# Optimization experiments

Measured on AMD Instinct MI355X. Metric: run time of the kernel, lower is better.

The kernel has to match this reference:

```python
import jax, jax.numpy as jnp
import numpy as np

B = 2
H = 256; Wd = 256; C = 128; S = 16        # image dims, channels, split_size
G = (H // S) * (Wd // S)                  # 256 heads (spatial groups)
N = S * S                                 # 256 patches per head
CI = C // 2                               # 64 channels per branch (gmlp input)
EI = 6                                    # inner gMLP expansion (MabGmlpBlock default e)
F1 = CI * EI                              # 384 = LocallyConnected expansion width
HF = F1 // 2                              # 192 = u/v split width
EPS = 1e-3                                # keras LayerNormalization default epsilon


def layer_norm(x, g, b):
    m = jnp.mean(x, axis=-1, keepdims=True)
    v = jnp.var(x, axis=-1, keepdims=True)
    return (x - m) * jax.lax.rsqrt(v + EPS) * g + b


def make_blocks(x):
    # 'B (H b1) (W b2) C -> B (H W) (b1 b2) C'
    b_, _, _, c_ = x.shape
    x = x.reshape(b_, H // S, S, Wd // S, S, c_)
    return x.transpose(0, 1, 3, 2, 4, 5).reshape(b_, G, N, c_)


def recon_blocks(x):
    # 'B (H W) (b1 b2) C -> B (H b1) (W b2) C'
    b_, _, _, c_ = x.shape
    x = x.reshape(b_, H // S, Wd // S, S, S, c_)
    return x.transpose(0, 1, 3, 2, 4, 5).reshape(b_, H, Wd, c_)


def recon_grids(x):
    # 'B (H W) (d1 d2) C -> B (d1 H) (d2 W) C'
    b_, _, _, c_ = x.shape
    x = x.reshape(b_, H // S, Wd // S, S, S, c_)
    return x.transpose(0, 3, 1, 4, 2, 5).reshape(b_, H, Wd, c_)


def gmlp(x, ln2_g, ln2_b, W1, b1, ln3_g, ln3_b, Wsgu, bsgu, W2, b2):
    # x: [B, G, N, CI]; all heads share weights -> batched einsum over (B, G)
    y = layer_norm(x, ln2_g, ln2_b)
    # LocallyConnected1D kernel_size=1: per-patch distinct weight [N, CI, F1]
    y = jax.nn.gelu(jnp.einsum('bgnc,ncf->bgnf', y, W1) + b1, approximate=False)
    u, v = jnp.split(y, 2, axis=-1)                      # [B,G,N,HF] each
    u = layer_norm(u, ln3_g, ln3_b)
    u = jnp.swapaxes(u, -1, -2)                          # [B,G,HF,N]
    # spatial gating: per-channel distinct [N->N] mixing, bias init ones
    u = jnp.einsum('bgcn,cnm->bgcm', u, Wsgu) + bsgu
    u = jnp.swapaxes(u, -1, -2)                          # [B,G,N,HF]
    return jnp.einsum('bgnc,ncf->bgnf', u * v, W2) + b2 + x


def setup_inputs() -> dict:
    key = jax.random.key(0)
    ks = jax.random.split(key, 8)
    x = jax.random.normal(ks[0], (B, H, Wd, C), jnp.float32)
    W_proj = jax.random.normal(ks[1], (C, C), jnp.float32) / np.sqrt(C).astype(np.float32)
    b_proj = jnp.zeros((C,), jnp.float32)
    W1 = jax.random.normal(ks[2], (N, CI, F1), jnp.float32) / np.sqrt(CI).astype(np.float32)
    b1 = jnp.zeros((N, F1), jnp.float32)
    Wsgu = jax.random.normal(ks[3], (HF, N, N), jnp.float32) * 0.001  # truncated_normal(0.001) approx
    bsgu = jnp.ones((HF, N), jnp.float32)                             # bias_initializer=ones
    W2 = jax.random.normal(ks[4], (N, HF, CI), jnp.float32) / np.sqrt(HF).astype(np.float32)
    b2 = jnp.zeros((N, CI), jnp.float32)
    return {
        'x': x,
        'ln1_g': jnp.ones((C,), jnp.float32), 'ln1_b': jnp.zeros((C,), jnp.float32),
        'W_proj': W_proj, 'b_proj': b_proj,
        'ln2_g': jnp.ones((CI,), jnp.float32), 'ln2_b': jnp.zeros((CI,), jnp.float32),
        'W1': W1, 'b1': b1,
        'ln3_g': jnp.ones((HF,), jnp.float32), 'ln3_b': jnp.zeros((HF,), jnp.float32),
        'Wsgu': Wsgu, 'bsgu': bsgu,
        'W2': W2, 'b2': b2,
    }


def reference(x, ln1_g, ln1_b, W_proj, b_proj, ln2_g, ln2_b, W1, b1,
              ln3_g, ln3_b, Wsgu, bsgu, W2, b2):
    y = layer_norm(x, ln1_g, ln1_b)
    y = jax.nn.gelu(y @ W_proj + b_proj, approximate=False)   # Dense(c*e), e=1
    local, glob = jnp.split(y, 2, axis=-1)                    # [B,H,W,CI] each
    g_args = (ln2_g, ln2_b, W1, b1, ln3_g, ln3_b, Wsgu, bsgu, W2, b2)
    local = recon_grids(gmlp(make_blocks(local), *g_args))    # multi-axis: block in, grid out
    glob = recon_blocks(gmlp(make_blocks(glob), *g_args))
    out = jnp.concatenate([local, glob], axis=-1) + x
    return out, glob
```

## Files before the change

kernel.cpp:

```cpp
#include <hip/hip_runtime.h>


typedef unsigned int uint_t;
typedef unsigned short us_t;
typedef __attribute__((ext_vector_type(8))) short bf16x8;
typedef __attribute__((ext_vector_type(4))) float f32x4;

#define EPSF 1e-3f

__device__ __forceinline__ float b2f(us_t h){ return __uint_as_float(((uint_t)h) << 16); }
__device__ __forceinline__ float lo2f(uint_t u){ return __uint_as_float(u << 16); }
__device__ __forceinline__ float hi2f(uint_t u){ return __uint_as_float(u & 0xFFFF0000u); }
__device__ __forceinline__ us_t f2b(float f){
  uint_t u = __float_as_uint(f);
  uint_t r = (u + 0x7FFFu + ((u >> 16) & 1u)) >> 16;
  return (us_t)r;
}
__device__ __forceinline__ uint_t pack2(float a, float b){
  return (uint_t)f2b(a) | ((uint_t)f2b(b) << 16);
}
__device__ __forceinline__ float gelu_f(float v){
  return 0.5f*v*(1.f + erff(v*0.7071067811865475f));
}

__global__ __launch_bounds__(256) void wprep(const float* __restrict__ Wsgu, us_t* __restrict__ WT){
  __shared__ us_t ls[64*264];
  int t = threadIdx.x;
  int c = blockIdx.x >> 2, kt = blockIdx.x & 3;
  const float* src = Wsgu + ((size_t)c*256 + kt*64)*256;
  #pragma unroll
  for (int i = 0; i < 16; i++){
    int chunk = i*256 + t;
    int kk = chunk >> 6, mm = (chunk & 63) << 2;
    float4 w = *(const float4*)(src + kk*256 + mm);
    *(uint2*)&ls[kk*264 + mm] = make_uint2(pack2(w.x,w.y), pack2(w.z,w.w));
  }
  __syncthreads();
  #pragma unroll
  for (int i = 0; i < 8; i++){
    int chunk = i*256 + t;
    int m = chunk >> 3, kk0 = (chunk & 7) << 3;
    const us_t* sp = &ls[kk0*264 + m];
    uint4 o;
    o.x = (uint_t)sp[0]     | ((uint_t)sp[264]   << 16);
    o.y = (uint_t)sp[2*264] | ((uint_t)sp[3*264] << 16);
    o.z = (uint_t)sp[4*264] | ((uint_t)sp[5*264] << 16);
    o.w = (uint_t)sp[6*264] | ((uint_t)sp[7*264] << 16);
    *(uint4*)(WT + ((size_t)c*256 + m)*256 + kt*64 + kk0) = o;
  }
}

__global__ __launch_bounds__(256) void k1_ln_proj(
    const float* __restrict__ x, const float* __restrict__ g1, const float* __restrict__ b1l,
    const float* __restrict__ Wp, const float* __restrict__ bp, us_t* __restrict__ xin)
{
  __shared__ __align__(16) float xs2[128*40];
  __shared__ __align__(16) us_t Ws[128*128];
  int t = threadIdx.x;
  int p0 = blockIdx.x * 32;

  {
    int pi = t >> 3, c0 = (t & 7) << 4;
    const float* src = x + (size_t)(p0 + pi)*128 + c0;
    float4 d0 = *(const float4*)src;
    float4 d1 = *(const float4*)(src + 4);
    float4 d2 = *(const float4*)(src + 8);
    float4 d3 = *(const float4*)(src + 12);
    float* dst = &xs2[c0*40 + pi];
    dst[0]   = d0.x; dst[40]  = d0.y; dst[80]  = d0.z; dst[120] = d0.w;
    dst[160] = d1.x; dst[200] = d1.y; dst[240] = d1.z; dst[280] = d1.w;
    dst[320] = d2.x; dst[360] = d2.y; dst[400] = d2.z; dst[440] = d2.w;
    dst[480] = d3.x; dst[520] = d3.y; dst[560] = d3.z; dst[600] = d3.w;
  }
  #pragma unroll
  for (int i = 0; i < 16; i++){
    int idx = (i*256 + t)*4;
    float4 w = *(const float4*)(Wp + idx);
    *(uint2*)&Ws[idx] = make_uint2(pack2(w.x,w.y), pack2(w.z,w.w));
  }
  __syncthreads();
  {
    int wv = t >> 6, ln = t & 63;
    float ga = g1[ln], gb = g1[ln+64];
    float ba = b1l[ln], bb = b1l[ln+64];
    for (int k = 0; k < 8; k++){
      int pi = wv*8 + k;
      float a = xs2[ln*40 + pi];
      float c = xs2[(ln+64)*40 + pi];
      float s = a + c, q = a*a + c*c;
      #pragma unroll
      for (int off = 32; off; off >>= 1){ s += __shfl_xor(s, off, 64); q += __shfl_xor(q, off, 64); }
      float m = s*(1.f/128.f);
      float rstd = rsqrtf(q*(1.f/128.f) - m*m + EPSF);
      xs2[ln*40 + pi]      = (a - m)*rstd*ga + ba;
      xs2[(ln+64)*40 + pi] = (c - m)*rstd*gb + bb;
    }
  }
  __syncthreads();
  int cg = t & 31, pg = t >> 5;
  int co0 = cg*4, p00 = pg*4;
  float acc[4][4] = {};
  #pragma unroll 4
  for (int ci = 0; ci < 128; ci++){
    float4 xv = *(const float4*)&xs2[ci*40 + p00];
    uint2 wv2 = *(const uint2*)&Ws[ci*128 + co0];
    float w0 = lo2f(wv2.x), w1 = hi2f(wv2.x), w2 = lo2f(wv2.y), w3 = hi2f(wv2.y);
    acc[0][0] += xv.x*w0; acc[0][1] += xv.x*w1; acc[0][2] += xv.x*w2; acc[0][3] += xv.x*w3;
    acc[1][0] += xv.y*w0; acc[1][1] += xv.y*w1; acc[1][2] += xv.y*w2; acc[1][3] += xv.y*w3;
    acc[2][0] += xv.z*w0; acc[2][1] += xv.z*w1; acc[2][2] += xv.z*w2; acc[2][3] += xv.z*w3;
    acc[3][0] += xv.w*w0; acc[3][1] += xv.w*w1; acc[3][2] += xv.w*w2; acc[3][3] += xv.w*w3;
  }
  float bb0 = bp[co0],   bb1 = bp[co0+1];
  float bb2 = bp[co0+2], bb3 = bp[co0+3];
  int branch = co0 >> 6;
  int c = co0 & 63;
  #pragma unroll
  for (int i = 0; i < 4; i++){
    int p = p0 + p00 + i;
    int b = p >> 16, rem = p & 65535, h = rem >> 8, w = rem & 255;
    int g = ((h >> 4) << 4) | (w >> 4);
    int nn = ((h & 15) << 4) | (w & 15);
    float y0 = gelu_f(acc[i][0] + bb0);
    float y1 = gelu_f(acc[i][1] + bb1);
    float y2 = gelu_f(acc[i][2] + bb2);
    float y3 = gelu_f(acc[i][3] + bb3);
    size_t row = (size_t)branch*512 + (size_t)b*256 + g;
    *(uint2*)(xin + (row*256 + nn)*64 + c) = make_uint2(pack2(y0,y1), pack2(y2,y3));
  }
}

__global__ __launch_bounds__(256) void k2_e1(
    const us_t* __restrict__ xin,
    const float* __restrict__ g2, const float* __restrict__ b2l,
    const float* __restrict__ W1, const float* __restrict__ b1v,
    const float* __restrict__ g3, const float* __restrict__ b3l,
    us_t* __restrict__ u_ln, us_t* __restrict__ vout, int r_base)
{
  __shared__ __align__(16) us_t Wl[64*384];
  __shared__ __align__(16) float xs2[64*36];
  __shared__ float b1s[384];
  int t = threadIdx.x;
  int n = blockIdx.x >> 2, rt = blockIdx.x & 3;

  const float* wsrc = W1 + (size_t)n*24576;
  #pragma unroll
  for (int i = 0; i < 24; i++){
    int idx = (i*256 + t)*4;
    float4 w = *(const float4*)(wsrc + idx);
    *(uint2*)&Wl[idx] = make_uint2(pack2(w.x,w.y), pack2(w.z,w.w));
  }
  if (t < 96){
    float4 d = *(const float4*)(b1v + n*384 + t*4);
    b1s[t*4+0] = d.x; b1s[t*4+1] = d.y; b1s[t*4+2] = d.z; b1s[t*4+3] = d.w;
  }
  {
    int rr = t >> 3, cc0 = (t & 7) << 3;
    uint4 d = *(const uint4*)(xin + ((size_t)(r_base + rt*32 + rr)*256 + n)*64 + cc0);
    float* dst = &xs2[cc0*36 + rr];
    dst[0]    = lo2f(d.x); dst[36]   = hi2f(d.x);
    dst[2*36] = lo2f(d.y); dst[3*36] = hi2f(d.y);
    dst[4*36] = lo2f(d.z); dst[5*36] = hi2f(d.z);
    dst[6*36] = lo2f(d.w); dst[7*36] = hi2f(d.w);
  }
  __syncthreads();
  {
    int wv = t >> 6, ln = t & 63;
    float gch = g2[ln], bch = b2l[ln];
    for (int k = 0; k < 8; k++){
      int row = wv*8 + k;
      float a = xs2[ln*36 + row];
      float s = a, q = a*a;
      #pragma unroll
      for (int off = 32; off; off >>= 1){ s += __shfl_xor(s, off, 64); q += __shfl_xor(q, off, 64); }
      float m = s*(1.f/64.f);
      float rstd = rsqrtf(q*(1.f/64.f) - m*m + EPSF);
      xs2[ln*36 + row] = (a - m)*rstd*gch + bch;
    }
  }
  __syncthreads();
  int fg = t & 31, rg = t >> 5;
  int f0 = fg*12, r00 = rg*4;
  float acc[4][12] = {};
  #pragma unroll 4
  for (int ci = 0; ci < 64; ci++){
    float4 xv = *(const float4*)&xs2[ci*36 + r00];
    const uint2* wp2 = (const uint2*)&Wl[ci*384 + f0];
    uint2 wa = wp2[0], wb = wp2[1], wc = wp2[2];
    float wf[12];
    wf[0]=lo2f(wa.x); wf[1]=hi2f(wa.x); wf[2]=lo2f(wa.y); wf[3]=hi2f(wa.y);
    wf[4]=lo2f(wb.x); wf[5]=hi2f(wb.x); wf[6]=lo2f(wb.y); wf[7]=hi2f(wb.y);
    wf[8]=lo2f(wc.x); wf[9]=hi2f(wc.x); wf[10]=lo2f(wc.y); wf[11]=hi2f(wc.y);
    float xa[4] = {xv.x, xv.y, xv.z, xv.w};
    #pragma unroll
    for (int i = 0; i < 4; i++)
      #pragma unroll
      for (int j = 0; j < 12; j++)
        acc[i][j] += xa[i]*wf[j];
  }
  bool isu = (fg < 16);
  float s4[4], q4[4];
  #pragma unroll
  for (int i = 0; i < 4; i++){
    float s = 0.f, q = 0.f;
    #pragma unroll
    for (int j = 0; j < 12; j++){
      float yv = gelu_f(acc[i][j] + b1s[f0 + j]);
      acc[i][j] = yv;
      s += yv; q += yv*yv;
    }
    s4[i] = isu ? s : 0.f;
    q4[i] = isu ? q : 0.f;
  }
  #pragma unroll
  for (int i = 0; i < 4; i++){
    float s = s4[i], q = q4[i];
    #pragma unroll
    for (int off = 16; off; off >>= 1){ s += __shfl_xor(s, off, 64); q += __shfl_xor(q, off, 64); }
    float m = s*(1.f/192.f);
    s4[i] = m;
    q4[i] = rsqrtf(q*(1.f/192.f) - m*m + EPSF);
  }
  if (isu){
    float gv[12], bv[12];
    #pragma unroll
    for (int j = 0; j < 12; j++){ gv[j] = g3[f0+j]; bv[j] = b3l[f0+j]; }
    #pragma unroll
    for (int i = 0; i < 4; i++){
      int r = rt*32 + r00 + i;
      float m = s4[i], rstd = q4[i];
      uint2* dst = (uint2*)(u_ln + ((size_t)r*256 + n)*192 + f0);
      uint2 o0, o1, o2;
      o0.x = pack2((acc[i][0]-m)*rstd*gv[0]+bv[0],  (acc[i][1]-m)*rstd*gv[1]+bv[1]);
      o0.y = pack2((acc[i][2]-m)*rstd*gv[2]+bv[2],  (acc[i][3]-m)*rstd*gv[3]+bv[3]);
      o1.x = pack2((acc[i][4]-m)*rstd*gv[4]+bv[4],  (acc[i][5]-m)*rstd*gv[5]+bv[5]);
      o1.y = pack2((acc[i][6]-m)*rstd*gv[6]+bv[6],  (acc[i][7]-m)*rstd*gv[7]+bv[7]);
      o2.x = pack2((acc[i][8]-m)*rstd*gv[8]+bv[8],  (acc[i][9]-m)*rstd*gv[9]+bv[9]);
      o2.y = pack2((acc[i][10]-m)*rstd*gv[10]+bv[10],(acc[i][11]-m)*rstd*gv[11]+bv[11]);
      dst[0] = o0; dst[1] = o1; dst[2] = o2;
    }
  } else {
    int fv0 = f0 - 192;
    #pragma unroll
    for (int i = 0; i < 4; i++){
      int r = rt*32 + r00 + i;
      uint2* dst = (uint2*)(vout + ((size_t)r*256 + n)*192 + fv0);
      uint2 o0, o1, o2;
      o0.x = pack2(acc[i][0], acc[i][1]);  o0.y = pack2(acc[i][2], acc[i][3]);
      o1.x = pack2(acc[i][4], acc[i][5]);  o1.y = pack2(acc[i][6], acc[i][7]);
      o2.x = pack2(acc[i][8], acc[i][9]);  o2.y = pack2(acc[i][10], acc[i][11]);
      dst[0] = o0; dst[1] = o1; dst[2] = o2;
    }
  }
}

__global__ __launch_bounds__(256) void t1_transpose(const us_t* __restrict__ u_ln, us_t* __restrict__ uT){
  __shared__ us_t ls[128*194];
  int t = threadIdx.x;
  int r = blockIdx.x >> 1, n0 = (blockIdx.x & 1) << 7;
  #pragma unroll
  for (int i = 0; i < 12; i++){
    int chunk = i*256 + t;
    int nn = chunk/24, c0 = (chunk - nn*24)*8;
    uint4 d = *(const uint4*)(u_ln + ((size_t)r*256 + n0 + nn)*192 + c0);
    us_t* dst = &ls[nn*194 + c0];
    dst[0] = (us_t)d.x; dst[1] = (us_t)(d.x>>16);
    dst[2] = (us_t)d.y; dst[3] = (us_t)(d.y>>16);
    dst[4] = (us_t)d.z; dst[5] = (us_t)(d.z>>16);
    dst[6] = (us_t)d.w; dst[7] = (us_t)(d.w>>16);
  }
  __syncthreads();
  #pragma unroll
  for (int i = 0; i < 12; i++){
    int chunk = i*256 + t;
    int c = chunk >> 4, nn0 = (chunk & 15) << 3;
    const us_t* sp = &ls[nn0*194 + c];
    uint4 o;
    o.x = (uint_t)sp[0]     | ((uint_t)sp[194]   << 16);
    o.y = (uint_t)sp[2*194] | ((uint_t)sp[3*194] << 16);
    o.z = (uint_t)sp[4*194] | ((uint_t)sp[5*194] << 16);
    o.w = (uint_t)sp[6*194] | ((uint_t)sp[7*194] << 16);
    *(uint4*)(uT + ((size_t)c*128 + r)*256 + n0 + nn0) = o;
  }
}

__global__ __launch_bounds__(256) void k3_sgu_mfma(
    const us_t* __restrict__ uT, const us_t* __restrict__ WT,
    const float* __restrict__ bsgu, us_t* __restrict__ sT)
{
  __shared__ __align__(16) us_t As[128*72];
  __shared__ __align__(16) us_t Bs[128*72];
  int t = threadIdx.x;
  int c = blockIdx.x >> 1, mt = blockIdx.x & 1;
  int lane = t & 63, wv = t >> 6;
  int wr0 = (wv >> 1) * 64, wm0 = (wv & 1) * 64;
  int fr = lane & 15, fq = lane >> 4;
  f32x4 acc[4][4] = {};

  const us_t* aSrc = uT + (size_t)c*128*256;
  const us_t* bSrc = WT + ((size_t)(c*256 + mt*128))*256;

  for (int ks = 0; ks < 256; ks += 64){
    #pragma unroll
    for (int i = 0; i < 4; i++){
      int chunk = i*256 + t;
      int rr = chunk >> 3, kk = (chunk & 7) << 3;
      *(uint4*)&As[rr*72 + kk] = *(const uint4*)(aSrc + rr*256 + ks + kk);
      *(uint4*)&Bs[rr*72 + kk] = *(const uint4*)(bSrc + rr*256 + ks + kk);
    }
    __syncthreads();
    #pragma unroll
    for (int s = 0; s < 2; s++){
      int kb = s*32 + fq*8;
      bf16x8 a[4], b[4];
      #pragma unroll
      for (int mi = 0; mi < 4; mi++)
        a[mi] = *(const bf16x8*)&As[(wr0 + mi*16 + fr)*72 + kb];
      #pragma unroll
      for (int ni = 0; ni < 4; ni++)
        b[ni] = *(const bf16x8*)&Bs[(wm0 + ni*16 + fr)*72 + kb];
      #pragma unroll
      for (int mi = 0; mi < 4; mi++)
        #pragma unroll
        for (int ni = 0; ni < 4; ni++)
          acc[mi][ni] = __builtin_amdgcn_mfma_f32_16x16x32_bf16(a[mi], b[ni], acc[mi][ni], 0, 0, 0);
    }
    __syncthreads();
  }
  float bsv[4];
  #pragma unroll
  for (int ni = 0; ni < 4; ni++)
    bsv[ni] = bsgu[c*256 + mt*128 + wm0 + ni*16 + fr];
  #pragma unroll
  for (int mi = 0; mi < 4; mi++){
    #pragma unroll
    for (int i = 0; i < 4; i++){
      int r = wr0 + mi*16 + fq*4 + i;
      us_t* dst = sT + ((size_t)c*128 + r)*256 + mt*128 + wm0 + fr;
      #pragma unroll
      for (int ni = 0; ni < 4; ni++)
        dst[ni*16] = f2b(acc[mi][ni][i] + bsv[ni]);
    }
  }
}

__global__ __launch_bounds__(256) void t2_mul(
    const us_t* __restrict__ sT, const us_t* __restrict__ v, us_t* __restrict__ tout)
{
  __shared__ us_t ls[192*130];
  int t = threadIdx.x;
  int r = blockIdx.x >> 1, m0 = (blockIdx.x & 1) << 7;
  #pragma unroll
  for (int i = 0; i < 12; i++){
    int chunk = i*256 + t;
    int c = chunk >> 4, mm0 = (chunk & 15) << 3;
    uint4 d = *(const uint4*)(sT + ((size_t)c*128 + r)*256 + m0 + mm0);
    us_t* dst = &ls[c*130 + mm0];
    dst[0] = (us_t)d.x; dst[1] = (us_t)(d.x>>16);
    dst[2] = (us_t)d.y; dst[3] = (us_t)(d.y>>16);
    dst[4] = (us_t)d.z; dst[5] = (us_t)(d.z>>16);
    dst[6] = (us_t)d.w; dst[7] = (us_t)(d.w>>16);
  }
  __syncthreads();
  #pragma unroll
  for (int i = 0; i < 12; i++){
    int chunk = i*256 + t;
    int mm = chunk/24, c0 = (chunk - mm*24)*8;
    size_t gidx = ((size_t)r*256 + m0 + mm)*192 + c0;
    uint4 vv = *(const uint4*)(v + gidx);
    const us_t* sp = &ls[c0*130 + mm];
    uint4 o;
    o.x = pack2(b2f(sp[0])*lo2f(vv.x),     b2f(sp[130])*hi2f(vv.x));
    o.y = pack2(b2f(sp[2*130])*lo2f(vv.y), b2f(sp[3*130])*hi2f(vv.y));
    o.z = pack2(b2f(sp[4*130])*lo2f(vv.z), b2f(sp[5*130])*hi2f(vv.z));
    o.w = pack2(b2f(sp[6*130])*lo2f(vv.w), b2f(sp[7*130])*hi2f(vv.w));
    *(uint4*)(tout + gidx) = o;
  }
}

__global__ __launch_bounds__(256) void k4_out(
    const us_t* __restrict__ tbuf, const float* __restrict__ W2,
    const float* __restrict__ b2v, const us_t* __restrict__ xin,
    const float* __restrict__ x, float* __restrict__ out0, float* __restrict__ out1,
    int r_base)
{
  __shared__ __align__(16) us_t W2s[192*64];
  __shared__ __align__(16) us_t ts[192*68];
  int t = threadIdx.x;
  int n = blockIdx.x >> 1, rt = blockIdx.x & 1;
  const float* wsrc = W2 + (size_t)n*12288;
  #pragma unroll
  for (int i = 0; i < 12; i++){
    int idx = (i*256 + t)*4;
    float4 w = *(const float4*)(wsrc + idx);
    *(uint2*)&W2s[idx] = make_uint2(pack2(w.x,w.y), pack2(w.z,w.w));
  }
  #pragma unroll
  for (int i = 0; i < 6; i++){
    int chunk = i*256 + t;
    int rr = chunk/24, ff0 = (chunk - rr*24)*8;
    uint4 d = *(const uint4*)(tbuf + ((size_t)(rt*64 + rr)*256 + n)*192 + ff0);
    us_t* dst = &ts[ff0*68 + rr];
    dst[0]    = (us_t)d.x; dst[68]   = (us_t)(d.x>>16);
    dst[2*68] = (us_t)d.y; dst[3*68] = (us_t)(d.y>>16);
    dst[4*68] = (us_t)d.z; dst[5*68] = (us_t)(d.z>>16);
    dst[6*68] = (us_t)d.w; dst[7*68] = (us_t)(d.w>>16);
  }
  __syncthreads();
  int cg = t & 15, rg = t >> 4;
  int c0 = cg*4, rr0 = rg*4;
  float acc[4][4] = {};
  #pragma unroll 4
  for (int f = 0; f < 192; f++){
    uint2 au = *(const uint2*)&ts[f*68 + rr0];
    uint2 wu = *(const uint2*)&W2s[f*64 + c0];
    float a0 = lo2f(au.x), a1 = hi2f(au.x), a2 = lo2f(au.y), a3 = hi2f(au.y);
    float w0 = lo2f(wu.x), w1 = hi2f(wu.x), w2 = lo2f(wu.y), w3 = hi2f(wu.y);
    acc[0][0] += a0*w0; acc[0][1] += a0*w1; acc[0][2] += a0*w2; acc[0][3] += a0*w3;
    acc[1][0] += a1*w0; acc[1][1] += a1*w1; acc[1][2] += a1*w2; acc[1][3] += a1*w3;
    acc[2][0] += a2*w0; acc[2][1] += a2*w1; acc[2][2] += a2*w2; acc[2][3] += a2*w3;
    acc[3][0] += a3*w0; acc[3][1] += a3*w1; acc[3][2] += a3*w2; acc[3][3] += a3*w3;
  }
  float4 bb = *(const float4*)(b2v + n*64 + c0);
  #pragma unroll
  for (int i = 0; i < 4; i++){
    int rl = rt*64 + rr0 + i;
    int r = r_base + rl;
    int branch = r >> 9, bidx = (r >> 8) & 1, g = r & 255;
    uint2 xi = *(const uint2*)(xin + ((size_t)r*256 + n)*64 + c0);
    float v0 = acc[i][0] + bb.x + lo2f(xi.x);
    float v1 = acc[i][1] + bb.y + hi2f(xi.x);
    float v2 = acc[i][2] + bb.z + lo2f(xi.y);
    float v3 = acc[i][3] + bb.w + hi2f(xi.y);
    int h, w;
    if (branch == 0){ h = ((n >> 4) << 4) | (g >> 4); w = ((n & 15) << 4) | (g & 15); }
    else            { h = ((g >> 4) << 4) | (n >> 4); w = ((g & 15) << 4) | (n & 15); }
    size_t base = (size_t)(bidx*256 + h)*256 + w;
    size_t o0idx = base*128 + (branch << 6) + c0;
    float4 xr = *(const float4*)(x + o0idx);
    *(float4*)(out0 + o0idx) = make_float4(v0 + xr.x, v1 + xr.y, v2 + xr.z, v3 + xr.w);
    if (branch){
      *(float4*)(out1 + base*64 + c0) = make_float4(v0, v1, v2, v3);
    }
  }
}

extern "C" void kernel_launch(void* const* d_in, const int* in_sizes, int n_in,
                              void* d_out, int out_size, void* d_ws, size_t ws_size,
                              hipStream_t stream)
{
  (void)in_sizes; (void)n_in; (void)out_size; (void)ws_size;
  const float* x    = (const float*)d_in[0];
  const float* g1   = (const float*)d_in[1];
  const float* b1l  = (const float*)d_in[2];
  const float* Wp   = (const float*)d_in[3];
  const float* bp   = (const float*)d_in[4];
  const float* g2   = (const float*)d_in[5];
  const float* b2l  = (const float*)d_in[6];
  const float* W1   = (const float*)d_in[7];
  const float* b1v  = (const float*)d_in[8];
  const float* g3   = (const float*)d_in[9];
  const float* b3l  = (const float*)d_in[10];
  const float* Wsgu = (const float*)d_in[11];
  const float* bsgu = (const float*)d_in[12];
  const float* W2   = (const float*)d_in[13];
  const float* b2v  = (const float*)d_in[14];

  float* out0 = (float*)d_out;
  float* out1 = out0 + (size_t)2*256*256*128;

  us_t* ws   = (us_t*)d_ws;
  us_t* xin  = ws;
  us_t* bufA = ws + 16777216;
  us_t* bufV = bufA + 6291456;
  us_t* bufB = bufV + 6291456;
  us_t* WT   = bufB + 6291456;

  wprep      <<<dim3(768),  dim3(256), 0, stream>>>(Wsgu, WT);
  k1_ln_proj <<<dim3(4096), dim3(256), 0, stream>>>(x, g1, b1l, Wp, bp, xin);
  for (int chunk = 0; chunk < 8; ++chunk){
    int r_base = chunk * 128;
    k2_e1       <<<dim3(1024), dim3(256), 0, stream>>>(xin, g2, b2l, W1, b1v, g3, b3l, bufA, bufV, r_base);
    t1_transpose<<<dim3(256),  dim3(256), 0, stream>>>(bufA, bufB);
    k3_sgu_mfma <<<dim3(384),  dim3(256), 0, stream>>>(bufB, WT, bsgu, bufA);
    t2_mul      <<<dim3(256),  dim3(256), 0, stream>>>(bufA, bufV, bufB);
    k4_out      <<<dim3(512),  dim3(256), 0, stream>>>(bufB, W2, b2v, xin, x, out0, out1, r_base);
  }
}
```

Before: 1.189 ms.

## Rewrite LN+projection kernel with bf16 MFMA and pre-transposed weights

The first-stage layernorm + Dense projection kernel moves from a scalar FMA loop to bf16 MFMA 16x16x32 instructions. Each block now handles 128 pixels instead of 32, so there are a quarter as many blocks. The projection weight is transposed and converted to bf16 once, by an extra block in the weight-prep kernel, instead of every block converting it. Layernorm stats are now computed in registers per thread pair, and normalized activations are stored to LDS as bf16, which adds rounding on the LN output.

New measurement: 1.178 ms. Within noise of the previous version (-0.9%).

```diff
diff --git a/kernel.cpp b/kernel.cpp
--- a/kernel.cpp
+++ b/kernel.cpp
@@ -23,9 +23,32 @@
   return 0.5f*v*(1.f + erff(v*0.7071067811865475f));
 }
 
-__global__ __launch_bounds__(256) void wprep(const float* __restrict__ Wsgu, us_t* __restrict__ WT){
-  __shared__ us_t ls[64*264];
-  int t = threadIdx.x;
+__global__ __launch_bounds__(256) void wprep(const float* __restrict__ Wsgu,
+                                             const float* __restrict__ Wp,
+                                             us_t* __restrict__ WT,
+                                             us_t* __restrict__ WpT){
+  __shared__ __align__(16) us_t ls[128*136];
+  int t = threadIdx.x;
+  if (blockIdx.x == 768){
+    #pragma unroll
+    for (int i = 0; i < 16; i++){
+      int idx = (i*256 + t)*4;
+      int row = idx >> 7, col = idx & 127;
+      float4 w = *(const float4*)(Wp + idx);
+      ls[(col+0)*136 + row] = f2b(w.x);
+      ls[(col+1)*136 + row] = f2b(w.y);
+      ls[(col+2)*136 + row] = f2b(w.z);
+      ls[(col+3)*136 + row] = f2b(w.w);
+    }
+    __syncthreads();
+    #pragma unroll
+    for (int i = 0; i < 8; i++){
+      int chunk = i*256 + t;
+      int o = chunk >> 4, i0 = (chunk & 15) << 3;
+      *(uint4*)(WpT + o*128 + i0) = *(const uint4*)&ls[o*136 + i0];
+    }
+    return;
+  }
   int c = blockIdx.x >> 2, kt = blockIdx.x & 3;
   const float* src = Wsgu + ((size_t)c*256 + kt*64)*256;
   #pragma unroll
@@ -52,80 +75,95 @@
 
 __global__ __launch_bounds__(256) void k1_ln_proj(
     const float* __restrict__ x, const float* __restrict__ g1, const float* __restrict__ b1l,
-    const float* __restrict__ Wp, const float* __restrict__ bp, us_t* __restrict__ xin)
+    const us_t* __restrict__ WpT, const float* __restrict__ bp, us_t* __restrict__ xin)
 {
-  __shared__ __align__(16) float xs2[128*40];
-  __shared__ __align__(16) us_t Ws[128*128];
-  int t = threadIdx.x;
-  int p0 = blockIdx.x * 32;
-
+  __shared__ __align__(16) us_t As[128*136];
+  __shared__ __align__(16) us_t Ws[128*136];
+  __shared__ float gs[128], bs[128];
+  int t = threadIdx.x;
+  int p0 = blockIdx.x * 128;
+  int lane = t & 63, wv = t >> 6;
+
+  if (t < 128){ gs[t] = g1[t]; bs[t] = b1l[t]; }
+  #pragma unroll
+  for (int i = 0; i < 8; i++){
+    int chunk = i*256 + t;
+    int row = chunk >> 4, k0 = (chunk & 15) << 3;
+    *(uint4*)&Ws[row*136 + k0] = *(const uint4*)(WpT + row*128 + k0);
+  }
+  int pl = t >> 1, half = t & 1;
+  const float* xr = x + (size_t)(p0 + pl)*128 + half*64;
+  float xv[64];
+  float s = 0.f, q = 0.f;
+  #pragma unroll
+  for (int i = 0; i < 16; i++){
+    float4 d = *(const float4*)(xr + i*4);
+    xv[i*4+0] = d.x; xv[i*4+1] = d.y; xv[i*4+2] = d.z; xv[i*4+3] = d.w;
+    s += d.x + d.y + d.z + d.w;
+    q += d.x*d.x + d.y*d.y + d.z*d.z + d.w*d.w;
+  }
+  s += __shfl_xor(s, 1, 64);
+  q += __shfl_xor(q, 1, 64);
+  float m = s*(1.f/128.f);
+  float rstd = rsqrtf(q*(1.f/128.f) - m*m + EPSF);
+  __syncthreads();
   {
-    int pi = t >> 3, c0 = (t & 7) << 4;
-    const float* src = x + (size_t)(p0 + pi)*128 + c0;
-    float4 d0 = *(const float4*)src;
-    float4 d1 = *(const float4*)(src + 4);
-    float4 d2 = *(const float4*)(src + 8);
-    float4 d3 = *(const float4*)(src + 12);
-    float* dst = &xs2[c0*40 + pi];
-    dst[0]   = d0.x; dst[40]  = d0.y; dst[80]  = d0.z; dst[120] = d0.w;
-    dst[160] = d1.x; dst[200] = d1.y; dst[240] = d1.z; dst[280] = d1.w;
-    dst[320] = d2.x; dst[360] = d2.y; dst[400] = d2.z; dst[440] = d2.w;
-    dst[480] = d3.x; dst[520] = d3.y; dst[560] = d3.z; dst[600] = d3.w;
-  }
-  #pragma unroll
-  for (int i = 0; i < 16; i++){
-    int idx = (i*256 + t)*4;
-    float4 w = *(const float4*)(Wp + idx);
-    *(uint2*)&Ws[idx] = make_uint2(pack2(w.x,w.y), pack2(w.z,w.w));
-  }
-  __syncthreads();
-  {
-    int wv = t >> 6, ln = t & 63;
-    float ga = g1[ln], gb = g1[ln+64];
-    float ba = b1l[ln], bb = b1l[ln+64];
-    for (int k = 0; k < 8; k++){
-      int pi = wv*8 + k;
-      float a = xs2[ln*40 + pi];
-      float c = xs2[(ln+64)*40 + pi];
-      float s = a + c, q = a*a + c*c;
-      #pragma unroll
-      for (int off = 32; off; off >>= 1){ s += __shfl_xor(s, off, 64); q += __shfl_xor(q, off, 64); }
-      float m = s*(1.f/128.f);
-      float rstd = rsqrtf(q*(1.f/128.f) - m*m + EPSF);
-      xs2[ln*40 + pi]      = (a - m)*rstd*ga + ba;
-      xs2[(ln+64)*40 + pi] = (c - m)*rstd*gb + bb;
-    }
-  }
-  __syncthreads();
-  int cg = t & 31, pg = t >> 5;
-  int co0 = cg*4, p00 = pg*4;
-  float acc[4][4] = {};
-  #pragma unroll 4
-  for (int ci = 0; ci < 128; ci++){
-    float4 xv = *(const float4*)&xs2[ci*40 + p00];
-    uint2 wv2 = *(const uint2*)&Ws[ci*128 + co0];
-    float w0 = lo2f(wv2.x), w1 = hi2f(wv2.x), w2 = lo2f(wv2.y), w3 = hi2f(wv2.y);
-    acc[0][0] += xv.x*w0; acc[0][1] += xv.x*w1; acc[0][2] += xv.x*w2; acc[0][3] += xv.x*w3;
-    acc[1][0] += xv.y*w0; acc[1][1] += xv.y*w1; acc[1][2] += xv.y*w2; acc[1][3] += xv.y*w3;
-    acc[2][0] += xv.z*w0; acc[2][1] += xv.z*w1; acc[2][2] += xv.z*w2; acc[2][3] += xv.z*w3;
-    acc[3][0] += xv.w*w0; acc[3][1] += xv.w*w1; acc[3][2] += xv.w*w2; acc[3][3] += xv.w*w3;
-  }
-  float bb0 = bp[co0],   bb1 = bp[co0+1];
-  float bb2 = bp[co0+2], bb3 = bp[co0+3];
-  int branch = co0 >> 6;
-  int c = co0 & 63;
-  #pragma unroll
-  for (int i = 0; i < 4; i++){
-    int p = p0 + p00 + i;
-    int b = p >> 16, rem = p & 65535, h = rem >> 8, w = rem & 255;
-    int g = ((h >> 4) << 4) | (w >> 4);
-    int nn = ((h & 15) << 4) | (w & 15);
-    float y0 = gelu_f(acc[i][0] + bb0);
-    float y1 = gelu_f(acc[i][1] + bb1);
-    float y2 = gelu_f(acc[i][2] + bb2);
-    float y3 = gelu_f(acc[i][3] + bb3);
-    size_t row = (size_t)branch*512 + (size_t)b*256 + g;
-    *(uint2*)(xin + (row*256 + nn)*64 + c) = make_uint2(pack2(y0,y1), pack2(y2,y3));
+    int c0 = half << 6;
+    us_t* dst = &As[pl*136 + c0];
+    #pragma unroll
+    for (int jj = 0; jj < 8; jj++){
+      float y[8];
+      #pragma unroll
+      for (int k = 0; k < 8; k++){
+        int idx = jj*8 + k;
+        y[k] = (xv[idx] - m)*rstd*gs[c0 + idx] + bs[c0 + idx];
+      }
+      uint4 o;
+      o.x = pack2(y[0], y[1]);
+      o.y = pack2(y[2], y[3]);
+      o.z = pack2(y[4], y[5]);
+      o.w = pack2(y[6], y[7]);
+      *(uint4*)&dst[jj*8] = o;
+    }
+  }
+  __syncthreads();
+  int wm0 = (wv >> 1) * 64, wn0 = (wv & 1) * 64;
+  int fr = lane & 15, fq = lane >> 4;
+  f32x4 acc[4][4] = {};
+  #pragma unroll
+  for (int sstep = 0; sstep < 4; sstep++){
+    int kb = sstep*32 + fq*8;
+    bf16x8 a[4], b[4];
+    #pragma unroll
+    for (int mi = 0; mi < 4; mi++)
+      a[mi] = *(const bf16x8*)&Ws[(wm0 + mi*16 + fr)*136 + kb];
+    #pragma unroll
+    for (int ni = 0; ni < 4; ni++)
+      b[ni] = *(const bf16x8*)&As[(wn0 + ni*16 + fr)*136 + kb];
+    #pragma unroll
+    for (int mi = 0; mi < 4; mi++)
+      #pragma unroll
+      for (int ni = 0; ni < 4; ni++)
+        acc[mi][ni] = __builtin_amdgcn_mfma_f32_16x16x32_bf16(a[mi], b[ni], acc[mi][ni], 0, 0, 0);
+  }
+  #pragma unroll
+  for (int mi = 0; mi < 4; mi++){
+    int ch0 = wm0 + mi*16 + fq*4;
+    float4 bb = *(const float4*)(bp + ch0);
+    int branch = ch0 >> 6, c = ch0 & 63;
+    #pragma unroll
+    for (int ni = 0; ni < 4; ni++){
+      int p = p0 + wn0 + ni*16 + fr;
+      int b_ = p >> 16, rem = p & 65535, h = rem >> 8, w = rem & 255;
+      int g = ((h >> 4) << 4) | (w >> 4);
+      int nn = ((h & 15) << 4) | (w & 15);
+      float v0 = gelu_f(acc[mi][ni][0] + bb.x);
+      float v1 = gelu_f(acc[mi][ni][1] + bb.y);
+      float v2 = gelu_f(acc[mi][ni][2] + bb.z);
+      float v3 = gelu_f(acc[mi][ni][3] + bb.w);
+      size_t row = (size_t)branch*512 + (size_t)b_*256 + g;
+      *(uint2*)(xin + (row*256 + nn)*64 + c) = make_uint2(pack2(v0,v1), pack2(v2,v3));
+    }
   }
 }
 
@@ -474,9 +512,10 @@
   us_t* bufV = bufA + 6291456;
   us_t* bufB = bufV + 6291456;
   us_t* WT   = bufB + 6291456;
-
-  wprep      <<<dim3(768),  dim3(256), 0, stream>>>(Wsgu, WT);
-  k1_ln_proj <<<dim3(4096), dim3(256), 0, stream>>>(x, g1, b1l, Wp, bp, xin);
+  us_t* WpT  = WT + 12582912;
+
+  wprep      <<<dim3(769),  dim3(256), 0, stream>>>(Wsgu, Wp, WT, WpT);
+  k1_ln_proj <<<dim3(1024), dim3(256), 0, stream>>>(x, g1, b1l, WpT, bp, xin);
   for (int chunk = 0; chunk < 8; ++chunk){
     int r_base = chunk * 128;
     k2_e1       <<<dim3(1024), dim3(256), 0, stream>>>(xin, g2, b2l, W1, b1v, g3, b3l, bufA, bufV, r_base);
```
